# Kernel optimization log

Measured on AMD Instinct MI355X. Metric: run time of the kernel, lower is better.

The kernel has to match this reference:

```python
import jax, jax.numpy as jnp
import numpy as np

B, T, E = 8, 2048, 1024  # batch, seq_len, emb_size (= output_emb_size)


def setup_inputs() -> dict:
    key = jax.random.key(0)
    k1, k2, k3, k4, k5, k6, k7 = jax.random.split(key, 7)
    return {
        "q": jax.random.normal(k1, (B, T, E), jnp.float32),
        "k": jax.random.normal(k2, (B, T, E), jnp.float32),
        "v": jax.random.normal(k3, (B, T, E), jnp.float32),
        "mask": jax.random.randint(k4, (T, T), 0, 2, jnp.int32),
        # nn.Linear weights, stored [out, in] as in torch; applied as x @ W.T
        "Wq": jax.random.normal(k5, (E, E), jnp.float32) / np.sqrt(E),
        "Wk": jax.random.normal(k6, (E, E), jnp.float32) / np.sqrt(E),
        "Wv": jax.random.normal(k7, (E, E), jnp.float32) / np.sqrt(E),
    }


def reference(q, k, v, mask, Wq, Wk, Wv):
    # QKV projections (bias-free Linear): x @ W.T
    query = jnp.einsum("bte,oe->bto", q, Wq)
    key_p = jnp.einsum("bse,oe->bso", k, Wk)
    value = jnp.einsum("bse,oe->bso", v, Wv)
    d = key_p.shape[-1]
    scores = jnp.einsum("bto,bso->bts", query, key_p) / np.sqrt(d).astype(jnp.float32)
    # torch.any(mask): mask is nonzero somewhere -> apply masked_fill(mask==0, -inf)
    scores = jnp.where(mask[None, :, :] == 0, -jnp.inf, scores)
    weights = jax.nn.softmax(scores, axis=-1)
    return jnp.einsum("bts,bso->bto", weights, value)
```

## Files before the change

### kernel.cpp

```cpp
#include <hip/hip_runtime.h>
#include <hip/hip_bf16.h>

typedef __attribute__((ext_vector_type(8))) short short8;
typedef __attribute__((ext_vector_type(8))) unsigned short ushortx8;
typedef __attribute__((ext_vector_type(4))) unsigned short ushortx4;
typedef __attribute__((ext_vector_type(4))) float floatx4;

#define NB 8
#define NT 2048
#define NE 1024

__device__ __forceinline__ unsigned short f2bf(float f){
  unsigned int u = __builtin_bit_cast(unsigned int, f);
  u += 0x7FFFu + ((u >> 16) & 1u);
  return (unsigned short)(u >> 16);
}
__device__ __forceinline__ float bf2f(unsigned short h){
  unsigned int u = ((unsigned int)h) << 16;
  return __builtin_bit_cast(float, u);
}

__device__ __forceinline__ void async16(void* lds, const void* g){
  __builtin_amdgcn_global_load_lds(
      (const __attribute__((address_space(1))) unsigned int*)g,
      (__attribute__((address_space(3))) unsigned int*)lds, 16, 0, 0);
}

#define MFMA16(d, va, vb) \
  d = __builtin_amdgcn_mfma_f32_16x16x32_bf16(va, vb, d, 0, 0, 0)

__global__ __launch_bounds__(256) void cvt3(const float* __restrict__ a0,
                                            const float* __restrict__ a1,
                                            const float* __restrict__ a2,
                                            unsigned short* __restrict__ out,
                                            int n4_per){
  const float* src = blockIdx.y == 0 ? a0 : (blockIdx.y == 1 ? a1 : a2);
  unsigned short* dst = out + (size_t)blockIdx.y * (size_t)n4_per * 4;
  int i = blockIdx.x * 256 + threadIdx.x;
  if (i < n4_per){
    floatx4 f = ((const floatx4*)src)[i];
    ushortx4 o;
    o.x = f2bf(f.x); o.y = f2bf(f.y); o.z = f2bf(f.z); o.w = f2bf(f.w);
    *(ushortx4*)(dst + (size_t)i * 4) = o;
  }
}

__global__ __launch_bounds__(256) void pack_mask(const int* __restrict__ m,
                                                 unsigned long long* __restrict__ bits){
  int t = blockIdx.x * 256 + threadIdx.x;
  const int4* p = (const int4*)(m + (size_t)t * 64);
  unsigned long long w = 0;
  #pragma unroll
  for (int jj = 0; jj < 16; jj++){
    int4 v = p[jj];
    w |= (unsigned long long)(v.x != 0) << (jj * 4 + 0);
    w |= (unsigned long long)(v.y != 0) << (jj * 4 + 1);
    w |= (unsigned long long)(v.z != 0) << (jj * 4 + 2);
    w |= (unsigned long long)(v.w != 0) << (jj * 4 + 3);
  }
  bits[t] = w;
}

template<int EPI>
__global__ __launch_bounds__(512, 2) void gemm_nt(
    const unsigned short* __restrict__ A, long strideA,
    const unsigned short* __restrict__ B, long strideB,
    void* __restrict__ Out, long strideOutBytes,
    const unsigned long long* __restrict__ mbits,
    int K, int gx, int gy)
{
  __shared__ __attribute__((aligned(16))) char Lds[131072];
  const int tid = threadIdx.x;
  const int lane = tid & 63, wave = tid >> 6;

  int L = blockIdx.x;
  int xcd = L & 7, tt = L >> 3;
  int x = tt % gx;
  int strip = xcd + ((tt / gx) << 3);
  int y = strip % gy, z = strip / gy;
  const int m0 = y << 8, n0 = x << 8;
  const int Nn = gx << 8;

  const unsigned short* Az = A + (size_t)z * strideA;
  const unsigned short* Bz = B + (size_t)z * strideB;

  const long rowb  = (long)K * 2;
  const long rs128 = rowb << 7;
  const int r0 = tid >> 2;
  const int c0 = (tid & 3) ^ ((r0 >> 1) & 3);
  const char* pA0 = (const char*)Az + (size_t)(m0 + r0) * rowb + (c0 << 4);
  const char* pA1 = pA0 + 64;
  const char* pB0 = (const char*)Bz + (size_t)(n0 + r0) * rowb + (c0 << 4);
  const char* pB1 = pB0 + 64;
  const int stg = tid << 4;

  auto stageU = [&](const char*& g, int ldsoff){
    async16(Lds + ldsoff + stg,        g);
    async16(Lds + ldsoff + stg + 8192, g + rs128);
    g += 128;
  };

  const int lm = lane & 15, qd = lane >> 4;
  const int wm = wave >> 2, wn = wave & 3;
  const int fsw  = (qd ^ ((lm >> 1) & 3)) << 4;
  const int aoff = ((wm << 7) + lm) * 64 + fsw;
  const int boff = 32768 + ((wn << 6) + lm) * 64 + fsw;

  floatx4 acc[8][4];
  floatx4 zero4 = {0.f, 0.f, 0.f, 0.f};
  #pragma unroll
  for (int a = 0; a < 8; a++)
    #pragma unroll
    for (int b = 0; b < 4; b++) acc[a][b] = zero4;

  const int NK = K >> 6;

  stageU(pB0, 32768);
  stageU(pA0, 0);
  stageU(pB1, 32768 + 16384);
  stageU(pA1, 16384);
  stageU(pB0, 65536 + 32768);
  stageU(pA0, 65536);
  stageU(pB1, 65536 + 32768 + 16384);
  asm volatile("s_waitcnt vmcnt(6)\n\ts_barrier" ::: "memory");

  short8 a[4], b[4];
  for (int t = 0; t < NK; ++t){
    const int rb = (t & 1) << 16;
    const int sb = rb ^ 65536;

    if (t + 1 < NK) stageU(pA1, sb + 16384);
    #pragma unroll
    for (int j = 0; j < 4; j++) a[j] = *(const short8*)(Lds + rb + aoff + j * 1024);
    #pragma unroll
    for (int n = 0; n < 4; n++) b[n] = *(const short8*)(Lds + rb + boff + n * 1024);
    asm volatile("s_waitcnt lgkmcnt(0)\n\ts_barrier" ::: "memory");
    __builtin_amdgcn_sched_barrier(0);
    __builtin_amdgcn_s_setprio(1);
    #pragma unroll
    for (int j = 0; j < 4; j++)
      #pragma unroll
      for (int n = 0; n < 4; n++) MFMA16(acc[j][n], a[j], b[n]);
    __builtin_amdgcn_s_setprio(0);

    if (t + 2 < NK) stageU(pB0, rb + 32768);
    #pragma unroll
    for (int j = 0; j < 4; j++) a[j] = *(const short8*)(Lds + rb + aoff + (4 + j) * 1024);
    asm volatile("s_waitcnt lgkmcnt(0)\n\ts_barrier" ::: "memory");
    __builtin_amdgcn_sched_barrier(0);
    __builtin_amdgcn_s_setprio(1);
    #pragma unroll
    for (int j = 0; j < 4; j++)
      #pragma unroll
      for (int n = 0; n < 4; n++) MFMA16(acc[4 + j][n], a[j], b[n]);
    __builtin_amdgcn_s_setprio(0);

    if (t + 2 < NK) stageU(pA0, rb);
    #pragma unroll
    for (int j = 0; j < 4; j++) a[j] = *(const short8*)(Lds + rb + 16384 + aoff + j * 1024);
    #pragma unroll
    for (int n = 0; n < 4; n++) b[n] = *(const short8*)(Lds + rb + 16384 + boff + n * 1024);
    asm volatile("s_waitcnt lgkmcnt(0)\n\ts_barrier" ::: "memory");
    __builtin_amdgcn_sched_barrier(0);
    __builtin_amdgcn_s_setprio(1);
    #pragma unroll
    for (int j = 0; j < 4; j++)
      #pragma unroll
      for (int n = 0; n < 4; n++) MFMA16(acc[j][n], a[j], b[n]);
    __builtin_amdgcn_s_setprio(0);

    if (t + 2 < NK) stageU(pB1, rb + 32768 + 16384);
    #pragma unroll
    for (int j = 0; j < 4; j++) a[j] = *(const short8*)(Lds + rb + 16384 + aoff + (4 + j) * 1024);
    if (t + 2 < NK)
      asm volatile("s_waitcnt vmcnt(6) lgkmcnt(0)\n\ts_barrier" ::: "memory");
    else
      asm volatile("s_waitcnt vmcnt(0) lgkmcnt(0)\n\ts_barrier" ::: "memory");
    __builtin_amdgcn_sched_barrier(0);
    __builtin_amdgcn_s_setprio(1);
    #pragma unroll
    for (int j = 0; j < 4; j++)
      #pragma unroll
      for (int n = 0; n < 4; n++) MFMA16(acc[4 + j][n], a[j], b[n]);
    __builtin_amdgcn_s_setprio(0);
  }

  char* OutZ = (char*)Out + (size_t)z * strideOutBytes;
  const int colbase = n0 + (wn << 6);
  if constexpr (EPI == 1){
    const int wcol = colbase >> 6;
    #pragma unroll
    for (int mi = 0; mi < 8; mi++){
      #pragma unroll
      for (int i = 0; i < 4; i++){
        int row = m0 + (wm << 7) + mi * 16 + qd * 4 + i;
        unsigned long long w = mbits[(size_t)row * (NT / 64) + wcol];
        unsigned short* po = (unsigned short*)OutZ + (size_t)row * Nn + colbase;
        #pragma unroll
        for (int ni = 0; ni < 4; ni++){
          float vv = acc[mi][ni][i];
          float s = ((w >> (ni * 16 + lm)) & 1ull) ? vv * 0.03125f : -INFINITY;
          po[ni * 16 + lm] = f2bf(s);
        }
      }
    }
  } else {
    #pragma unroll
    for (int mi = 0; mi < 8; mi++){
      #pragma unroll
      for (int i = 0; i < 4; i++){
        int row = m0 + (wm << 7) + mi * 16 + qd * 4 + i;
        #pragma unroll
        for (int ni = 0; ni < 4; ni++){
          int col = colbase + ni * 16 + lm;
          float vv = acc[mi][ni][i];
          if constexpr (EPI == 0)
            ((unsigned short*)OutZ)[(size_t)row * Nn + col] = f2bf(vv);
          else
            ((float*)OutZ)[(size_t)row * Nn + col] = vv;
        }
      }
    }
  }
}

__global__ __launch_bounds__(256) void transpose_bf16(const unsigned short* __restrict__ in,
                                                      unsigned short* __restrict__ out,
                                                      int rows, int cols){
  __shared__ __attribute__((aligned(16))) unsigned short tile[64][72];
  const unsigned short* ib = in + (size_t)blockIdx.z * rows * cols;
  unsigned short* ob = out + (size_t)blockIdx.z * rows * cols;
  int r0 = blockIdx.x * 64;
  int c0 = blockIdx.y * 64;
  int tid = threadIdx.x;
  #pragma unroll
  for (int i = 0; i < 2; i++){
    int id = tid + i * 256;
    int r = id >> 3, c = (id & 7) * 8;
    ushortx8 v = *(const ushortx8*)(ib + (size_t)(r0 + r) * cols + c0 + c);
    *(ushortx8*)&tile[r][c] = v;
  }
  __syncthreads();
  #pragma unroll
  for (int i = 0; i < 2; i++){
    int id = tid + i * 256;
    int r = id >> 3, c = (id & 7) * 8;
    ushortx8 v;
    #pragma unroll
    for (int j = 0; j < 8; j++) v[j] = tile[c + j][r];
    *(ushortx8*)(ob + (size_t)(c0 + r) * rows + r0 + c) = v;
  }
}

__global__ __launch_bounds__(256) void softmax_rows(unsigned short* __restrict__ S){
  size_t row = blockIdx.x;
  unsigned short* p = S + row * NT;
  int tid = threadIdx.x;
  ushortx8 v = *(const ushortx8*)(p + tid * 8);
  float f[8];
  #pragma unroll
  for (int j = 0; j < 8; j++) f[j] = bf2f(v[j]);
  float mx = f[0];
  #pragma unroll
  for (int j = 1; j < 8; j++) mx = fmaxf(mx, f[j]);
  #pragma unroll
  for (int off = 32; off > 0; off >>= 1) mx = fmaxf(mx, __shfl_xor(mx, off, 64));
  __shared__ float redm[4], reds[4];
  int lane = tid & 63, wv = tid >> 6;
  if (lane == 0) redm[wv] = mx;
  __syncthreads();
  mx = fmaxf(fmaxf(redm[0], redm[1]), fmaxf(redm[2], redm[3]));
  float e[8]; float se = 0.f;
  #pragma unroll
  for (int j = 0; j < 8; j++){ e[j] = __expf(f[j] - mx); se += e[j]; }
  #pragma unroll
  for (int off = 32; off > 0; off >>= 1) se += __shfl_xor(se, off, 64);
  if (lane == 0) reds[wv] = se;
  __syncthreads();
  se = reds[0] + reds[1] + reds[2] + reds[3];
  float inv = 1.f / se;
  ushortx8 o;
  #pragma unroll
  for (int j = 0; j < 8; j++) o[j] = f2bf(e[j] * inv);
  *(ushortx8*)(p + tid * 8) = o;
}

extern "C" void kernel_launch(void* const* d_in, const int* in_sizes, int n_in,
                              void* d_out, int out_size, void* d_ws, size_t ws_size,
                              hipStream_t stream){
  const float* q  = (const float*)d_in[0];
  const float* k  = (const float*)d_in[1];
  const float* v  = (const float*)d_in[2];
  const int* mask = (const int*)d_in[3];
  const float* Wq = (const float*)d_in[4];
  const float* Wk = (const float*)d_in[5];
  const float* Wv = (const float*)d_in[6];

  const size_t BTE = (size_t)NB * NT * NE;
  unsigned short* ws   = (unsigned short*)d_ws;
  unsigned short* QKVp = ws;
  unsigned short* VpT  = ws + 3 * BTE;
  unsigned short* Sb   = ws + 3 * BTE + BTE;
  unsigned short* Qin  = ws + 3 * BTE;
  unsigned short* Wb   = ws + 3 * BTE + BTE + (size_t)NB * NT * NT;
  unsigned long long* mbits = (unsigned long long*)(Wb + (size_t)3 * NE * NE);

  unsigned short* Qp = QKVp;
  unsigned short* Kp = QKVp + BTE;
  unsigned short* Vp = QKVp + 2 * BTE;

  cvt3<<<dim3(16384, 3), 256, 0, stream>>>(q, k, v, Qin, (int)(BTE / 4));
  cvt3<<<dim3(1024, 3), 256, 0, stream>>>(Wq, Wk, Wv, Wb, NE * NE / 4);
  pack_mask<<<256, 256, 0, stream>>>(mask, mbits);

  gemm_nt<0><<<768, 512, 0, stream>>>(
      Qin, (long)BTE, Wb, (long)NE * NE,
      QKVp, (long)BTE * 2, nullptr, NE, 4, 64);

  transpose_bf16<<<dim3(32, 16, 8), 256, 0, stream>>>(Vp, VpT, NT, NE);

  gemm_nt<1><<<512, 512, 0, stream>>>(
      Qp, (long)NT * NE, Kp, (long)NT * NE,
      Sb, (long)NT * NT * 2, mbits, NE, 8, 8);

  softmax_rows<<<dim3(NB * NT), 256, 0, stream>>>(Sb);

  gemm_nt<2><<<256, 512, 0, stream>>>(
      Sb, (long)NT * NT, VpT, (long)NE * NT,
      d_out, (long)NT * NE * 4, nullptr, NT, 4, 8);
}
```

Baseline: 499.9 us.

## Fuse softmax into score GEMM epilogue and defer normalization to PV GEMM

Removes the standalone softmax kernel. The QK^T epilogue now writes unnormalized exp(score) in bf16 and accumulates per-row sums into a small buffer with atomics; the buffer is zeroed inside the transpose kernel. The PV GEMM epilogue divides each output row by its row sum. This saves a full read and write of the score matrix. It drops the max subtraction, so it relies on the scores being small enough that exp does not overflow. Separately, the GEMM main loop is reordered so LDS reads are issued before the async global stages, with barriers split around the MFMA blocks.

```diff
diff --git a/kernel.cpp b/kernel.cpp
--- a/kernel.cpp
+++ b/kernel.cpp
@@ -67,6 +67,7 @@
     const unsigned short* __restrict__ B, long strideB,
     void* __restrict__ Out, long strideOutBytes,
     const unsigned long long* __restrict__ mbits,
+    float* __restrict__ rowsums,
     int K, int gx, int gy)
 {
   __shared__ __attribute__((aligned(16))) char Lds[131072];
@@ -129,12 +130,13 @@
     const int rb = (t & 1) << 16;
     const int sb = rb ^ 65536;
 
+    #pragma unroll
+    for (int j = 0; j < 4; j++) a[j] = *(const short8*)(Lds + rb + aoff + j * 1024);
+    #pragma unroll
+    for (int n = 0; n < 4; n++) b[n] = *(const short8*)(Lds + rb + boff + n * 1024);
     if (t + 1 < NK) stageU(pA1, sb + 16384);
-    #pragma unroll
-    for (int j = 0; j < 4; j++) a[j] = *(const short8*)(Lds + rb + aoff + j * 1024);
-    #pragma unroll
-    for (int n = 0; n < 4; n++) b[n] = *(const short8*)(Lds + rb + boff + n * 1024);
-    asm volatile("s_waitcnt lgkmcnt(0)\n\ts_barrier" ::: "memory");
+    __builtin_amdgcn_s_barrier();
+    asm volatile("s_waitcnt lgkmcnt(0)" ::: "memory");
     __builtin_amdgcn_sched_barrier(0);
     __builtin_amdgcn_s_setprio(1);
     #pragma unroll
@@ -142,11 +144,13 @@
       #pragma unroll
       for (int n = 0; n < 4; n++) MFMA16(acc[j][n], a[j], b[n]);
     __builtin_amdgcn_s_setprio(0);
-
+    __builtin_amdgcn_s_barrier();
+
+    #pragma unroll
+    for (int j = 0; j < 4; j++) a[j] = *(const short8*)(Lds + rb + aoff + (4 + j) * 1024);
     if (t + 2 < NK) stageU(pB0, rb + 32768);
-    #pragma unroll
-    for (int j = 0; j < 4; j++) a[j] = *(const short8*)(Lds + rb + aoff + (4 + j) * 1024);
-    asm volatile("s_waitcnt lgkmcnt(0)\n\ts_barrier" ::: "memory");
+    __builtin_amdgcn_s_barrier();
+    asm volatile("s_waitcnt lgkmcnt(0)" ::: "memory");
     __builtin_amdgcn_sched_barrier(0);
     __builtin_amdgcn_s_setprio(1);
     #pragma unroll
@@ -154,13 +158,15 @@
       #pragma unroll
       for (int n = 0; n < 4; n++) MFMA16(acc[4 + j][n], a[j], b[n]);
     __builtin_amdgcn_s_setprio(0);
-
+    __builtin_amdgcn_s_barrier();
+
+    #pragma unroll
+    for (int j = 0; j < 4; j++) a[j] = *(const short8*)(Lds + rb + 16384 + aoff + j * 1024);
+    #pragma unroll
+    for (int n = 0; n < 4; n++) b[n] = *(const short8*)(Lds + rb + 16384 + boff + n * 1024);
     if (t + 2 < NK) stageU(pA0, rb);
-    #pragma unroll
-    for (int j = 0; j < 4; j++) a[j] = *(const short8*)(Lds + rb + 16384 + aoff + j * 1024);
-    #pragma unroll
-    for (int n = 0; n < 4; n++) b[n] = *(const short8*)(Lds + rb + 16384 + boff + n * 1024);
-    asm volatile("s_waitcnt lgkmcnt(0)\n\ts_barrier" ::: "memory");
+    __builtin_amdgcn_s_barrier();
+    asm volatile("s_waitcnt lgkmcnt(0)" ::: "memory");
     __builtin_amdgcn_sched_barrier(0);
     __builtin_amdgcn_s_setprio(1);
     #pragma unroll
@@ -168,14 +174,18 @@
       #pragma unroll
       for (int n = 0; n < 4; n++) MFMA16(acc[j][n], a[j], b[n]);
     __builtin_amdgcn_s_setprio(0);
-
-    if (t + 2 < NK) stageU(pB1, rb + 32768 + 16384);
+    __builtin_amdgcn_s_barrier();
+
     #pragma unroll
     for (int j = 0; j < 4; j++) a[j] = *(const short8*)(Lds + rb + 16384 + aoff + (4 + j) * 1024);
-    if (t + 2 < NK)
-      asm volatile("s_waitcnt vmcnt(6) lgkmcnt(0)\n\ts_barrier" ::: "memory");
-    else
-      asm volatile("s_waitcnt vmcnt(0) lgkmcnt(0)\n\ts_barrier" ::: "memory");
+    if (t + 2 < NK){
+      stageU(pB1, rb + 32768 + 16384);
+      asm volatile("s_waitcnt vmcnt(6)" ::: "memory");
+    } else {
+      asm volatile("s_waitcnt vmcnt(0)" ::: "memory");
+    }
+    __builtin_amdgcn_s_barrier();
+    asm volatile("s_waitcnt lgkmcnt(0)" ::: "memory");
     __builtin_amdgcn_sched_barrier(0);
     __builtin_amdgcn_s_setprio(1);
     #pragma unroll
@@ -183,6 +193,7 @@
       #pragma unroll
       for (int n = 0; n < 4; n++) MFMA16(acc[4 + j][n], a[j], b[n]);
     __builtin_amdgcn_s_setprio(0);
+    __builtin_amdgcn_s_barrier();
   }
 
   char* OutZ = (char*)Out + (size_t)z * strideOutBytes;
@@ -196,11 +207,32 @@
         int row = m0 + (wm << 7) + mi * 16 + qd * 4 + i;
         unsigned long long w = mbits[(size_t)row * (NT / 64) + wcol];
         unsigned short* po = (unsigned short*)OutZ + (size_t)row * Nn + colbase;
+        float rsum = 0.f;
         #pragma unroll
         for (int ni = 0; ni < 4; ni++){
           float vv = acc[mi][ni][i];
-          float s = ((w >> (ni * 16 + lm)) & 1ull) ? vv * 0.03125f : -INFINITY;
-          po[ni * 16 + lm] = f2bf(s);
+          float e = ((w >> (ni * 16 + lm)) & 1ull) ? __expf(vv * 0.03125f) : 0.f;
+          rsum += e;
+          po[ni * 16 + lm] = f2bf(e);
+        }
+        rsum += __shfl_xor(rsum, 1, 64);
+        rsum += __shfl_xor(rsum, 2, 64);
+        rsum += __shfl_xor(rsum, 4, 64);
+        rsum += __shfl_xor(rsum, 8, 64);
+        if (lm == 0) atomicAdd(rowsums + ((size_t)z << 11) + row, rsum);
+      }
+    }
+  } else if constexpr (EPI == 2){
+    #pragma unroll
+    for (int mi = 0; mi < 8; mi++){
+      #pragma unroll
+      for (int i = 0; i < 4; i++){
+        int row = m0 + (wm << 7) + mi * 16 + qd * 4 + i;
+        float inv = 1.0f / rowsums[((size_t)z << 11) + row];
+        #pragma unroll
+        for (int ni = 0; ni < 4; ni++){
+          int col = colbase + ni * 16 + lm;
+          ((float*)OutZ)[(size_t)row * Nn + col] = acc[mi][ni][i] * inv;
         }
       }
     }
@@ -213,11 +245,7 @@
         #pragma unroll
         for (int ni = 0; ni < 4; ni++){
           int col = colbase + ni * 16 + lm;
-          float vv = acc[mi][ni][i];
-          if constexpr (EPI == 0)
-            ((unsigned short*)OutZ)[(size_t)row * Nn + col] = f2bf(vv);
-          else
-            ((float*)OutZ)[(size_t)row * Nn + col] = vv;
+          ((unsigned short*)OutZ)[(size_t)row * Nn + col] = f2bf(acc[mi][ni][i]);
         }
       }
     }
@@ -226,6 +254,7 @@
 
 __global__ __launch_bounds__(256) void transpose_bf16(const unsigned short* __restrict__ in,
                                                       unsigned short* __restrict__ out,
+                                                      float* __restrict__ rowsums,
                                                       int rows, int cols){
   __shared__ __attribute__((aligned(16))) unsigned short tile[64][72];
   const unsigned short* ib = in + (size_t)blockIdx.z * rows * cols;
@@ -233,6 +262,11 @@
   int r0 = blockIdx.x * 64;
   int c0 = blockIdx.y * 64;
   int tid = threadIdx.x;
+  if (blockIdx.x == 0 && blockIdx.y == 0){
+    float* rz = rowsums + ((size_t)blockIdx.z << 11);
+    #pragma unroll
+    for (int i = 0; i < 8; i++) rz[tid + i * 256] = 0.f;
+  }
   #pragma unroll
   for (int i = 0; i < 2; i++){
     int id = tid + i * 256;
@@ -250,39 +284,6 @@
     for (int j = 0; j < 8; j++) v[j] = tile[c + j][r];
     *(ushortx8*)(ob + (size_t)(c0 + r) * rows + r0 + c) = v;
   }
-}
-
-__global__ __launch_bounds__(256) void softmax_rows(unsigned short* __restrict__ S){
-  size_t row = blockIdx.x;
-  unsigned short* p = S + row * NT;
-  int tid = threadIdx.x;
-  ushortx8 v = *(const ushortx8*)(p + tid * 8);
-  float f[8];
-  #pragma unroll
-  for (int j = 0; j < 8; j++) f[j] = bf2f(v[j]);
-  float mx = f[0];
-  #pragma unroll
-  for (int j = 1; j < 8; j++) mx = fmaxf(mx, f[j]);
-  #pragma unroll
-  for (int off = 32; off > 0; off >>= 1) mx = fmaxf(mx, __shfl_xor(mx, off, 64));
-  __shared__ float redm[4], reds[4];
-  int lane = tid & 63, wv = tid >> 6;
-  if (lane == 0) redm[wv] = mx;
-  __syncthreads();
-  mx = fmaxf(fmaxf(redm[0], redm[1]), fmaxf(redm[2], redm[3]));
-  float e[8]; float se = 0.f;
-  #pragma unroll
-  for (int j = 0; j < 8; j++){ e[j] = __expf(f[j] - mx); se += e[j]; }
-  #pragma unroll
-  for (int off = 32; off > 0; off >>= 1) se += __shfl_xor(se, off, 64);
-  if (lane == 0) reds[wv] = se;
-  __syncthreads();
-  se = reds[0] + reds[1] + reds[2] + reds[3];
-  float inv = 1.f / se;
-  ushortx8 o;
-  #pragma unroll
-  for (int j = 0; j < 8; j++) o[j] = f2bf(e[j] * inv);
-  *(ushortx8*)(p + tid * 8) = o;
 }
 
 extern "C" void kernel_launch(void* const* d_in, const int* in_sizes, int n_in,
@@ -304,6 +305,7 @@
   unsigned short* Qin  = ws + 3 * BTE;
   unsigned short* Wb   = ws + 3 * BTE + BTE + (size_t)NB * NT * NT;
   unsigned long long* mbits = (unsigned long long*)(Wb + (size_t)3 * NE * NE);
+  float* rowsums = (float*)Wb;
 
   unsigned short* Qp = QKVp;
   unsigned short* Kp = QKVp + BTE;
@@ -315,17 +317,15 @@
 
   gemm_nt<0><<<768, 512, 0, stream>>>(
       Qin, (long)BTE, Wb, (long)NE * NE,
-      QKVp, (long)BTE * 2, nullptr, NE, 4, 64);
-
-  transpose_bf16<<<dim3(32, 16, 8), 256, 0, stream>>>(Vp, VpT, NT, NE);
+      QKVp, (long)BTE * 2, nullptr, nullptr, NE, 4, 64);
+
+  transpose_bf16<<<dim3(32, 16, 8), 256, 0, stream>>>(Vp, VpT, rowsums, NT, NE);
 
   gemm_nt<1><<<512, 512, 0, stream>>>(
       Qp, (long)NT * NE, Kp, (long)NT * NE,
-      Sb, (long)NT * NT * 2, mbits, NE, 8, 8);
-
-  softmax_rows<<<dim3(NB * NT), 256, 0, stream>>>(Sb);
+      Sb, (long)NT * NT * 2, mbits, rowsums, NE, 8, 8);
 
   gemm_nt<2><<<256, 512, 0, stream>>>(
       Sb, (long)NT * NT, VpT, (long)NE * NT,
-      d_out, (long)NT * NE * 4, nullptr, NT, 4, 8);
-}
+      d_out, (long)NT * NE * 4, nullptr, rowsums, NT, 4, 8);
+}
```

After: 508.1 us. No clear change (+1.6%).
